# Kernel tuning notes

Measured on AMD Instinct MI355X. Metric: run time of the kernel, lower is better.

## Reference

```python
import jax, jax.numpy as jnp
import numpy as np

NEG = -1.0e9

def setup_inputs() -> dict:
    key = jax.random.key(0)
    k1, k2 = jax.random.split(key)
    B, S, D = 4, 4096, 256
    encodings = jax.random.normal(k1, (B, S, D), dtype=jnp.float32)
    # nn.Linear weight [out, in]; Linear applies x @ W.T
    W = jax.random.normal(k2, (D, D), dtype=jnp.float32) * (1.0 / np.sqrt(D))
    return {"encodings": encodings, "W": W}

def reference(encodings, W):
    B, S, D = encodings.shape
    enc_mult_W = jnp.einsum('bsd,ed->bse', encodings, W)          # Linear, no bias
    sims = jnp.einsum('bqd,bkd->bqk', encodings, enc_mult_W)       # E @ (EW^T)^T
    scaled = sims / jnp.asarray(np.sqrt(D), dtype=sims.dtype)
    # causal mask: positions k > q masked out (top-left softmax == 1)
    mask = jnp.triu(jnp.ones((S, S), dtype=bool), k=1)
    scaled = jnp.where(mask[None, :, :], jnp.asarray(NEG, scaled.dtype), scaled)
    attn = jax.nn.softmax(scaled, axis=-1)
    return jnp.einsum('bqk,bkd->bqd', attn, encodings)
```

## Files before the change

### kernel.cpp

```cpp
#include <hip/hip_runtime.h>
#include <hip/hip_bf16.h>
#include <cstdint>
#include <cstddef>

typedef __attribute__((ext_vector_type(4))) float f32x4;
typedef __attribute__((ext_vector_type(8))) short s16x8;
typedef __attribute__((ext_vector_type(4))) unsigned int u32x4;

#define SDIM 4096
#define DDIM 256

#define GLOAD_LDS16(g, s)                                                      \
  __builtin_amdgcn_global_load_lds(                                            \
      (const __attribute__((address_space(1))) void*)(g),                      \
      (__attribute__((address_space(3))) void*)(s), 16, 0, 0)

__device__ __forceinline__ unsigned short cvt_bf16(float f) {
  union { float f; unsigned int u; } v;
  v.f = f;
  unsigned int u = v.u;
  unsigned int r = (u + 0x7FFFu + ((u >> 16) & 1u)) >> 16;
  return (unsigned short)r;
}

__device__ __forceinline__ float bf2f(unsigned short s) {
  union { unsigned int u; float f; } v;
  v.u = ((unsigned int)s) << 16;
  return v.f;
}

__global__ __launch_bounds__(256) void k_convw(const float* __restrict__ W,
                                               unsigned short* __restrict__ Wb) {
  int i = (blockIdx.x * 256 + threadIdx.x) * 8;
  f32x4 a = *(const f32x4*)(W + i);
  f32x4 b = *(const f32x4*)(W + i + 4);
  s16x8 o;
#pragma unroll
  for (int j = 0; j < 4; ++j) {
    o[j] = (short)cvt_bf16(a[j]);
    o[4 + j] = (short)cvt_bf16(b[j]);
  }
  *(s16x8*)(Wb + i) = o;
}

__global__ __launch_bounds__(256) void k_transv(const float* __restrict__ E,
                                                unsigned short* __restrict__ Vt) {
  __shared__ float tile[64][65];
  const int tid = threadIdx.x;
  const int b = blockIdx.z;
  const int s0 = blockIdx.x * 64, d0 = blockIdx.y * 64;
  const int tx = tid & 63, ty = tid >> 6;
#pragma unroll
  for (int i = 0; i < 16; ++i) {
    int sr = i * 4 + ty;
    tile[sr][tx] = E[((size_t)(b * SDIM) + s0 + sr) * DDIM + d0 + tx];
  }
  __syncthreads();
#pragma unroll
  for (int i = 0; i < 16; ++i) {
    int dr = i * 4 + ty;
    Vt[((size_t)(b * DDIM) + d0 + dr) * SDIM + s0 + tx] = cvt_bf16(tile[tx][dr]);
  }
}

__global__ __launch_bounds__(256) void k_proj(const float* __restrict__ E,
                                              const unsigned short* __restrict__ Wb,
                                              unsigned short* __restrict__ Kp) {
  const int tid = threadIdx.x;
  const int w = tid >> 6, l = tid & 63, lhi = l >> 4, llo = l & 15;
  const int m0 = blockIdx.x * 64 + w * 16;
  f32x4 acc[16];
#pragma unroll
  for (int n = 0; n < 16; ++n) acc[n] = (f32x4){0.f, 0.f, 0.f, 0.f};
  const float* arow = E + (size_t)(m0 + llo) * DDIM;
#pragma unroll
  for (int kd = 0; kd < 8; ++kd) {
    const int dbase = kd * 32 + lhi * 8;
    f32x4 a0 = *(const f32x4*)(arow + dbase);
    f32x4 a1 = *(const f32x4*)(arow + dbase + 4);
    s16x8 af;
#pragma unroll
    for (int j = 0; j < 4; ++j) {
      af[j] = (short)cvt_bf16(a0[j]);
      af[4 + j] = (short)cvt_bf16(a1[j]);
    }
#pragma unroll
    for (int n = 0; n < 16; ++n) {
      s16x8 bf = *(const s16x8*)(Wb + (n * 16 + llo) * DDIM + dbase);
      acc[n] = __builtin_amdgcn_mfma_f32_16x16x32_bf16(af, bf, acc[n], 0, 0, 0);
    }
  }
  const float sc = 1.4426950408889634f / 16.0f;
#pragma unroll
  for (int n = 0; n < 16; ++n) {
#pragma unroll
    for (int r = 0; r < 4; ++r) {
      Kp[(size_t)(m0 + lhi * 4 + r) * DDIM + n * 16 + llo] = cvt_bf16(acc[n][r] * sc);
    }
  }
}

__global__ __launch_bounds__(256, 2) void k_attn(const float* __restrict__ E,
                                                 const unsigned short* __restrict__ Kp,
                                                 const unsigned short* __restrict__ Vt,
                                                 unsigned short* __restrict__ Po,
                                                 float* __restrict__ Lp, int nch) {
  __shared__ u32x4 smem4[4736];
  char* smem = (char*)smem4;
  const int tid = threadIdx.x;
  const int l = tid & 63, w = tid >> 6, lhi = l >> 4, llo = l & 15;
  const int half = 64 * nch;
  const int h = blockIdx.x / half;
  const int i0 = blockIdx.x % half;
  const int b = i0 / (16 * nch);
  const int j0 = i0 % (16 * nch);
  const int rq = j0 / nch;
  const int ch = j0 % nch;
  const int qt = h ? rq : 31 - rq;
  const int q0 = qt * 128;
  const int nst = (qt + 1) * (4 / nch);
  const int step0 = ch * nst;
  const int wq0 = q0 + w * 32;

  s16x8 qf[2][8];
#pragma unroll
  for (int s = 0; s < 2; ++s) {
    const float* Eq = E + ((size_t)(b * SDIM) + wq0 + s * 16 + llo) * DDIM;
#pragma unroll
    for (int kd = 0; kd < 8; ++kd) {
      f32x4 a0 = *(const f32x4*)(Eq + kd * 32 + lhi * 8);
      f32x4 a1 = *(const f32x4*)(Eq + kd * 32 + lhi * 8 + 4);
#pragma unroll
      for (int j = 0; j < 4; ++j) {
        qf[s][kd][j] = (short)cvt_bf16(a0[j]);
        qf[s][kd][4 + j] = (short)cvt_bf16(a1[j]);
      }
    }
  }

  f32x4 oT[2][16];
#pragma unroll
  for (int s = 0; s < 2; ++s)
#pragma unroll
    for (int n = 0; n < 16; ++n) oT[s][n] = (f32x4){0.f, 0.f, 0.f, 0.f};
  float lsum[2] = {0.f, 0.f};

  const int trow = tid >> 5;
  const int kcolb = ((tid & 31) << 4) ^ ((trow & 7) << 4);
  const char* KpB = (const char*)Kp + (size_t)b * SDIM * 512;
  const char* VtB = (const char*)Vt + (size_t)b * DDIM * (SDIM * 2);

  auto stage = [&](int t) {
    const int kv0 = (step0 + t) * 32;
    char* kdst = smem + ((t & 1) * 16384);
    char* vdst = smem + 32768 + ((t & 1) * 16384);
    const char* ks = KpB + (size_t)(kv0 + trow) * 512 + kcolb;
    const char* vs = VtB + (size_t)tid * (SDIM * 2) + (size_t)kv0 * 2;
#pragma unroll
    for (int i = 0; i < 4; ++i)
      GLOAD_LDS16(ks + (size_t)i * 4096, kdst + i * 4096 + tid * 16);
#pragma unroll
    for (int i = 0; i < 4; ++i)
      GLOAD_LDS16(vs + i * 16, vdst + i * 4096 + tid * 16);
  };

  stage(0);
  char* sPw = smem + 65536 + w * 2560;

  for (int t = 0; t < nst; ++t) {
    const int kv0 = (step0 + t) * 32;
    const char* kb_ = smem + ((t & 1) * 16384);
    const char* vb_ = smem + 32768 + ((t & 1) * 16384);

    __syncthreads();
    if (t + 1 < nst) stage(t + 1);

#pragma unroll
    for (int kb = 0; kb < 2; ++kb) {
      f32x4 sa0 = (f32x4){0.f, 0.f, 0.f, 0.f};
      f32x4 sa1 = (f32x4){0.f, 0.f, 0.f, 0.f};
      const char* krow = kb_ + (kb * 16 + llo) * 512;
      __builtin_amdgcn_s_setprio(1);
#pragma unroll
      for (int kd = 0; kd < 8; ++kd) {
        s16x8 kf = *(const s16x8*)(krow + ((kd * 64 + lhi * 16) ^ ((llo & 7) << 4)));
        sa0 = __builtin_amdgcn_mfma_f32_16x16x32_bf16(kf, qf[0][kd], sa0, 0, 0, 0);
        sa1 = __builtin_amdgcn_mfma_f32_16x16x32_bf16(kf, qf[1][kd], sa1, 0, 0, 0);
      }
      __builtin_amdgcn_s_setprio(0);
      const int kvr = kv0 + kb * 16 + lhi * 4;
#pragma unroll
      for (int s = 0; s < 2; ++s) {
        const f32x4 sa = s ? sa1 : sa0;
        const int qi = wq0 + s * 16 + llo;
        float p[4];
#pragma unroll
        for (int rr = 0; rr < 4; ++rr) {
          float v = exp2f(sa[rr] - 32.0f);
          p[rr] = (kvr + rr > qi) ? 0.0f : v;
        }
        lsum[s] += (p[0] + p[1]) + (p[2] + p[3]);
        unsigned int w0 = __builtin_amdgcn_perm(__float_as_uint(p[1]),
                                                __float_as_uint(p[0]), 0x07060302u);
        unsigned int w1 = __builtin_amdgcn_perm(__float_as_uint(p[3]),
                                                __float_as_uint(p[2]), 0x07060302u);
        *(uint2*)(sPw + (s * 16 + llo) * 80 + kb * 32 + lhi * 8) = make_uint2(w0, w1);
      }
    }

    s16x8 pb0 = *(const s16x8*)(sPw + llo * 80 + lhi * 16);
    s16x8 pb1 = *(const s16x8*)(sPw + (16 + llo) * 80 + lhi * 16);
    __builtin_amdgcn_s_setprio(1);
#pragma unroll
    for (int n = 0; n < 16; ++n) {
      s16x8 vf = *(const s16x8*)(vb_ + lhi * 4096 + (n * 16 + llo) * 16);
      oT[0][n] = __builtin_amdgcn_mfma_f32_16x16x32_bf16(vf, pb0, oT[0][n], 0, 0, 0);
      oT[1][n] = __builtin_amdgcn_mfma_f32_16x16x32_bf16(vf, pb1, oT[1][n], 0, 0, 0);
    }
    __builtin_amdgcn_s_setprio(0);
  }

#pragma unroll
  for (int s = 0; s < 2; ++s) {
    lsum[s] += __shfl_xor(lsum[s], 16);
    lsum[s] += __shfl_xor(lsum[s], 32);
  }
  const int chb = ch * 4 + b;
#pragma unroll
  for (int s = 0; s < 2; ++s) {
    const int q = wq0 + s * 16 + llo;
    unsigned short* PoW = Po + ((size_t)chb * SDIM + q) * DDIM;
#pragma unroll
    for (int n = 0; n < 16; ++n) {
      unsigned int w0 =
          (unsigned int)cvt_bf16(oT[s][n][0]) | ((unsigned int)cvt_bf16(oT[s][n][1]) << 16);
      unsigned int w1 =
          (unsigned int)cvt_bf16(oT[s][n][2]) | ((unsigned int)cvt_bf16(oT[s][n][3]) << 16);
      *(uint2*)(PoW + n * 16 + lhi * 4) = make_uint2(w0, w1);
    }
    if (lhi == 0) Lp[(size_t)chb * SDIM + q] = lsum[s];
  }
}

__global__ __launch_bounds__(256) void k_merge(const unsigned short* __restrict__ Po,
                                               const float* __restrict__ Lp,
                                               float* __restrict__ out, int nch) {
  const size_t e = ((size_t)blockIdx.x * 256 + threadIdx.x) * 8;
  const size_t f = e >> 8;
  float lt = 0.f;
  for (int c = 0; c < nch; ++c) lt += Lp[(size_t)c * 16384 + f];
  const float inv = 1.0f / lt;
  float acc[8] = {0.f, 0.f, 0.f, 0.f, 0.f, 0.f, 0.f, 0.f};
  for (int c = 0; c < nch; ++c) {
    s16x8 a = *(const s16x8*)(Po + (size_t)c * 4194304 + e);
#pragma unroll
    for (int j = 0; j < 8; ++j) acc[j] += bf2f((unsigned short)a[j]);
  }
  f32x4 o0, o1;
#pragma unroll
  for (int j = 0; j < 4; ++j) {
    o0[j] = acc[j] * inv;
    o1[j] = acc[4 + j] * inv;
  }
  *(f32x4*)(out + e) = o0;
  *(f32x4*)(out + e + 4) = o1;
}

extern "C" void kernel_launch(void* const* d_in, const int* in_sizes, int n_in,
                              void* d_out, int out_size, void* d_ws, size_t ws_size,
                              hipStream_t stream) {
  (void)in_sizes; (void)n_in; (void)out_size;
  const float* E = (const float*)d_in[0];
  const float* W = (const float*)d_in[1];
  float* out = (float*)d_out;
  char* ws = (char*)d_ws;

  const size_t need4 = 16777216ull + 4ull * 8388608ull + 262144ull + 131072ull + 1048576ull;
  const int nch = (ws_size >= need4) ? 4 : 2;

  unsigned short* Kp = (unsigned short*)(ws);
  unsigned short* Vt = (unsigned short*)(ws + 8388608);
  unsigned short* Po = (unsigned short*)(ws + 16777216);
  size_t lp_off = 16777216ull + (size_t)nch * 8388608ull;
  float* Lp = (float*)(ws + lp_off);
  unsigned short* Wb = (unsigned short*)(ws + lp_off + 262144);

  k_convw<<<dim3(32), dim3(256), 0, stream>>>(W, Wb);
  k_transv<<<dim3(64, 4, 4), dim3(256), 0, stream>>>(E, Vt);
  k_proj<<<dim3(256), dim3(256), 0, stream>>>(E, Wb, Kp);
  k_attn<<<dim3(128 * nch), dim3(256), 0, stream>>>(E, Kp, Vt, Po, Lp, nch);
  k_merge<<<dim3(2048), dim3(256), 0, stream>>>(Po, Lp, out, nch);
}
```

Before: 129.8 us.

## Interleave KV splits across chunks and allow eight-way split-K attention

Split-K attention now hands out KV tiles round-robin (tile ch + nch*t) instead of contiguous ranges, so every chunk of a query tile gets about the same amount of causal work. Blocks are ordered heaviest query tile first, and an eight-way split is used when the workspace is large enough. Chunks that get no tiles write zeros for their partial output and row sums. The V tile staging layout is also changed to match the interleaved 32-column loads. This adds merge traffic and partial-output memory as the split count grows.

Measured after the change: 126.3 us. 1.03x faster.

```diff
diff --git a/kernel.cpp b/kernel.cpp
--- a/kernel.cpp
+++ b/kernel.cpp
@@ -109,18 +109,23 @@
   char* smem = (char*)smem4;
   const int tid = threadIdx.x;
   const int l = tid & 63, w = tid >> 6, lhi = l >> 4, llo = l & 15;
-  const int half = 64 * nch;
-  const int h = blockIdx.x / half;
-  const int i0 = blockIdx.x % half;
-  const int b = i0 / (16 * nch);
-  const int j0 = i0 % (16 * nch);
-  const int rq = j0 / nch;
-  const int ch = j0 % nch;
-  const int qt = h ? rq : 31 - rq;
+  const int u = blockIdx.x % (4 * nch);
+  const int t_ = blockIdx.x / (4 * nch);
+  const int qt = 31 - t_;
+  const int b = u & 3, ch = u >> 2;
   const int q0 = qt * 128;
-  const int nst = (qt + 1) * (4 / nch);
-  const int step0 = ch * nst;
+  const int chb = ch * 4 + b;
+  const int nst = (4 * (qt + 1) - ch + nch - 1) / nch;
   const int wq0 = q0 + w * 32;
+
+  if (4 * (qt + 1) <= ch) {
+    char* Pz = (char*)(Po + ((size_t)chb * SDIM + q0) * DDIM);
+    const u32x4 z = (u32x4){0u, 0u, 0u, 0u};
+#pragma unroll
+    for (int i = 0; i < 16; ++i) *(u32x4*)(Pz + tid * 256 + i * 16) = z;
+    if (tid < 128) Lp[(size_t)chb * SDIM + q0 + tid] = 0.f;
+    return;
+  }
 
   s16x8 qf[2][8];
 #pragma unroll
@@ -149,26 +154,27 @@
   const int kcolb = ((tid & 31) << 4) ^ ((trow & 7) << 4);
   const char* KpB = (const char*)Kp + (size_t)b * SDIM * 512;
   const char* VtB = (const char*)Vt + (size_t)b * DDIM * (SDIM * 2);
+  const char* vsb = VtB + (size_t)(tid >> 2) * 8192 + (size_t)((tid & 3) * 8) * 2;
 
   auto stage = [&](int t) {
-    const int kv0 = (step0 + t) * 32;
+    const int kv0 = (ch + nch * t) * 32;
     char* kdst = smem + ((t & 1) * 16384);
     char* vdst = smem + 32768 + ((t & 1) * 16384);
     const char* ks = KpB + (size_t)(kv0 + trow) * 512 + kcolb;
-    const char* vs = VtB + (size_t)tid * (SDIM * 2) + (size_t)kv0 * 2;
+    const char* vs = vsb + (size_t)kv0 * 2;
 #pragma unroll
     for (int i = 0; i < 4; ++i)
       GLOAD_LDS16(ks + (size_t)i * 4096, kdst + i * 4096 + tid * 16);
 #pragma unroll
     for (int i = 0; i < 4; ++i)
-      GLOAD_LDS16(vs + i * 16, vdst + i * 4096 + tid * 16);
+      GLOAD_LDS16(vs + (size_t)i * (64 * 8192), vdst + i * 4096 + tid * 16);
   };
 
   stage(0);
   char* sPw = smem + 65536 + w * 2560;
 
   for (int t = 0; t < nst; ++t) {
-    const int kv0 = (step0 + t) * 32;
+    const int kv0 = (ch + nch * t) * 32;
     const char* kb_ = smem + ((t & 1) * 16384);
     const char* vb_ = smem + 32768 + ((t & 1) * 16384);
 
@@ -213,7 +219,7 @@
     __builtin_amdgcn_s_setprio(1);
 #pragma unroll
     for (int n = 0; n < 16; ++n) {
-      s16x8 vf = *(const s16x8*)(vb_ + lhi * 4096 + (n * 16 + llo) * 16);
+      s16x8 vf = *(const s16x8*)(vb_ + (n * 16 + llo) * 64 + lhi * 16);
       oT[0][n] = __builtin_amdgcn_mfma_f32_16x16x32_bf16(vf, pb0, oT[0][n], 0, 0, 0);
       oT[1][n] = __builtin_amdgcn_mfma_f32_16x16x32_bf16(vf, pb1, oT[1][n], 0, 0, 0);
     }
@@ -225,7 +231,6 @@
     lsum[s] += __shfl_xor(lsum[s], 16);
     lsum[s] += __shfl_xor(lsum[s], 32);
   }
-  const int chb = ch * 4 + b;
 #pragma unroll
   for (int s = 0; s < 2; ++s) {
     const int q = wq0 + s * 16 + llo;
@@ -275,19 +280,24 @@
   float* out = (float*)d_out;
   char* ws = (char*)d_ws;
 
-  const size_t need4 = 16777216ull + 4ull * 8388608ull + 262144ull + 131072ull + 1048576ull;
-  const int nch = (ws_size >= need4) ? 4 : 2;
+  const size_t base = 16777216ull;
+  auto need = [&](int c) {
+    return base + (size_t)c * 8388608ull + (size_t)c * 65536ull + 262144ull;
+  };
+  int nch = 2;
+  if (ws_size >= need(8)) nch = 8;
+  else if (ws_size >= need(4)) nch = 4;
 
   unsigned short* Kp = (unsigned short*)(ws);
   unsigned short* Vt = (unsigned short*)(ws + 8388608);
-  unsigned short* Po = (unsigned short*)(ws + 16777216);
-  size_t lp_off = 16777216ull + (size_t)nch * 8388608ull;
+  unsigned short* Po = (unsigned short*)(ws + base);
+  size_t lp_off = base + (size_t)nch * 8388608ull;
   float* Lp = (float*)(ws + lp_off);
-  unsigned short* Wb = (unsigned short*)(ws + lp_off + 262144);
+  unsigned short* Wb = (unsigned short*)(ws + lp_off + (size_t)nch * 65536ull);
 
   k_convw<<<dim3(32), dim3(256), 0, stream>>>(W, Wb);
   k_transv<<<dim3(64, 4, 4), dim3(256), 0, stream>>>(E, Vt);
   k_proj<<<dim3(256), dim3(256), 0, stream>>>(E, Wb, Kp);
-  k_attn<<<dim3(128 * nch), dim3(256), 0, stream>>>(E, Kp, Vt, Po, Lp, nch);
+  k_attn<<<dim3(32 * 4 * nch), dim3(256), 0, stream>>>(E, Kp, Vt, Po, Lp, nch);
   k_merge<<<dim3(2048), dim3(256), 0, stream>>>(Po, Lp, out, nch);
 }
```
